# Kernel optimization log

Hardware: AMD Instinct MI355X
Metric: run time of the kernel (lower is better)

The kernel has to match this reference:

```python
import jax, jax.numpy as jnp
import numpy as np

NUM_CODES = 1024
CODE_DIM = 256
TEMPERATURE = 1.0  # forward default, clamped to >= 0.01 in original


def setup_inputs() -> dict:
    key = jax.random.key(0)
    k_z, k_e = jax.random.split(key)
    z = jax.random.normal(k_z, (16, 4096, CODE_DIM), dtype=jnp.float32)
    # embed buffer initialized as randn * 0.5 in the torch module
    embed = jax.random.normal(k_e, (NUM_CODES, CODE_DIM), dtype=jnp.float32) * 0.5
    return {"z": z, "embed": embed}


def reference(z, embed):
    K, D = embed.shape
    orig_shape = z.shape
    flat_z = z.reshape(-1, D)                      # [B, D]
    B = flat_z.shape[0]

    dist = (
        jnp.sum(flat_z * flat_z, axis=1, keepdims=True)
        - 2.0 * (flat_z @ embed.T)
        + jnp.sum(embed * embed, axis=1)[None, :]
    )

    soft_assign = jax.nn.softmax(-dist / max(TEMPERATURE, 0.01), axis=-1)  # [B, K]
    codes = jnp.argmin(dist, axis=1)               # [B]
    z_q = embed[codes]                             # [B, D] gather

    sg = jax.lax.stop_gradient
    commitment_loss = jnp.mean((flat_z - sg(z_q)) ** 2)
    codebook_loss = jnp.mean((z_q - sg(flat_z)) ** 2)

    avg_soft = jnp.mean(soft_assign, axis=0)       # [K]
    usage_entropy = -jnp.sum(avg_soft * jnp.log(avg_soft + 1e-10))
    diversity_loss = -usage_entropy / np.log(K).astype(np.float32)

    # straight-through estimator
    z_q_st = (flat_z + sg(z_q - flat_z)).reshape(orig_shape)
    codes_out = codes.reshape(orig_shape[:-1])

    # hard usage / perplexity (scatter-add instead of BxK one-hot)
    counts = jnp.zeros((K,), dtype=jnp.float32).at[codes].add(1.0)
    hard_avg = counts / jnp.asarray(B, dtype=jnp.float32)
    perplexity = jnp.exp(-jnp.sum(hard_avg * jnp.log(hard_avg + 1e-10)))

    return (z_q_st, codes_out, commitment_loss, codebook_loss,
            diversity_loss, usage_entropy, perplexity)
```

## Files before the change

kernel.cpp:

```cpp
#include <hip/hip_runtime.h>
#include <math.h>

typedef _Float16 half8 __attribute__((ext_vector_type(8)));
typedef float f32x4 __attribute__((ext_vector_type(4)));

#define AS1 __attribute__((address_space(1)))
#define AS3 __attribute__((address_space(3)))

#define BTOT   65536
#define DDIM   256
#define KC     1024

__global__ void vq_e2(const float* __restrict__ embed, float* __restrict__ e2g) {
    int gt = blockIdx.x * blockDim.x + threadIdx.x;
    int k = gt >> 6;
    int lane = gt & 63;
    float4 v = *(const float4*)(embed + (size_t)k * DDIM + lane * 4);
    float s = v.x * v.x + v.y * v.y + v.z * v.z + v.w * v.w;
    #pragma unroll
    for (int off = 1; off < 64; off <<= 1) s += __shfl_xor(s, off);
    if (lane == 0) e2g[k] = s;
}

__global__ void vq_prep(const float* __restrict__ embed, char* __restrict__ wsB) {
    int id = blockIdx.x * 256 + threadIdx.x;
    int c  = id >> 5;
    int kc = (id >> 2) & 7;
    int s  = id & 3;
    const float* src = embed + (size_t)c * DDIM + kc * 32 + s * 8;
    half8 hi, lo;
    #pragma unroll
    for (int j = 0; j < 8; ++j) {
        float xv = src[j];
        _Float16 hh = (_Float16)xv;
        hi[j] = hh;
        lo[j] = (_Float16)(xv - (float)hh);
    }
    int h = c >> 9, cl = c & 511;
    int inner = cl * 64 + ((s ^ (c & 3)) << 4);
    *(half8*)(wsB + (size_t)(kc * 4 + h) * 32768 + inner) = hi;
    *(half8*)(wsB + (size_t)(kc * 4 + 2 + h) * 32768 + inner) = lo;
}

__global__ __launch_bounds__(512, 2)
void vq_main(const float* __restrict__ z, const char* __restrict__ wsB,
             const float* __restrict__ e2g, float* __restrict__ psum_g,
             float* __restrict__ counts_g, float* __restrict__ distsum_g,
             float* __restrict__ codes_f_out)
{
    __shared__ __align__(16) char ldsA[65536];
    __shared__ __align__(16) char ldsB[2][32768];
    __shared__ float psum_lds[KC];
    __shared__ float lmax[64][8];
    __shared__ int   larg[64][8];
    __shared__ float lsum[64][8];
    __shared__ float rowM[64];
    __shared__ float rowInv[64];
    __shared__ float z2row[64];

    const int tid  = threadIdx.x;
    const int w    = tid >> 6;
    const int lane = tid & 63;
    const int row0 = blockIdx.x * 64;
    const int bA = (lane & 15) * 64 + (((lane >> 4) ^ (lane & 3)) << 4);

    psum_lds[tid] = 0.f;
    psum_lds[tid + 512] = 0.f;

    {
        const int ar = tid >> 3;
        const int kc = tid & 7;
        const float* src = z + (size_t)(row0 + ar) * DDIM + kc * 32;
        float x[32];
        #pragma unroll
        for (int j = 0; j < 8; ++j) {
            float4 v = ((const float4*)src)[j];
            x[4*j] = v.x; x[4*j+1] = v.y; x[4*j+2] = v.z; x[4*j+3] = v.w;
        }
        float zsq = 0.f;
        #pragma unroll
        for (int j = 0; j < 32; ++j) zsq = fmaf(x[j], x[j], zsq);
        zsq += __shfl_xor(zsq, 1);
        zsq += __shfl_xor(zsq, 2);
        zsq += __shfl_xor(zsq, 4);
        if ((tid & 7) == 0) z2row[ar] = zsq;
        #pragma unroll
        for (int s = 0; s < 4; ++s) {
            half8 hi, lo;
            #pragma unroll
            for (int j = 0; j < 8; ++j) {
                float xv = x[8*s + j];
                _Float16 hh = (_Float16)xv;
                hi[j] = hh;
                lo[j] = (_Float16)(xv - (float)hh);
            }
            int off = kc * 4096 + ar * 64 + ((s ^ (ar & 3)) << 4);
            *(half8*)(ldsA + off) = hi;
            *(half8*)(ldsA + 32768 + off) = lo;
        }
    }
    {
        const char* gs = wsB + tid * 16;
        char* ld = &ldsB[0][tid * 16];
        #pragma unroll
        for (int r = 0; r < 4; ++r)
            __builtin_amdgcn_global_load_lds((AS1 const void*)(gs + r * 8192),
                                             (AS3 void*)(ld + r * 8192), 16, 0, 0);
    }
    __syncthreads();

    f32x4 acc[4][8];
    #pragma unroll
    for (int rt = 0; rt < 4; ++rt)
        #pragma unroll
        for (int cg = 0; cg < 8; ++cg)
            acc[rt][cg] = (f32x4){0.f, 0.f, 0.f, 0.f};

    half8 aHi[4], aLo[4];

    #pragma unroll
    for (int kc = 0; kc < 8; ++kc) {
        #pragma unroll
        for (int p = 0; p < 2; ++p) {
            #pragma unroll
            for (int h = 0; h < 2; ++h) {
                const int s = kc * 4 + p * 2 + h;
                asm volatile("s_waitcnt vmcnt(0)\n\ts_barrier" ::: "memory");
                if (s + 1 < 32) {
                    const char* gs = wsB + (size_t)(s + 1) * 32768 + tid * 16;
                    char* ld = &ldsB[(s + 1) & 1][tid * 16];
                    #pragma unroll
                    for (int r = 0; r < 4; ++r)
                        __builtin_amdgcn_global_load_lds((AS1 const void*)(gs + r * 8192),
                                                         (AS3 void*)(ld + r * 8192), 16, 0, 0);
                }
                if (p == 0 && h == 0) {
                    #pragma unroll
                    for (int rt = 0; rt < 4; ++rt) {
                        aHi[rt] = *(const half8*)(ldsA + kc * 4096 + rt * 1024 + bA);
                        aLo[rt] = *(const half8*)(ldsA + 32768 + kc * 4096 + rt * 1024 + bA);
                    }
                }
                const char* bb = &ldsB[s & 1][w * 4096 + bA];
                #pragma unroll
                for (int ct = 0; ct < 4; ++ct) {
                    half8 bf = *(const half8*)(bb + ct * 1024);
                    const int cg = h * 4 + ct;
                    #pragma unroll
                    for (int rt = 0; rt < 4; ++rt) {
                        acc[rt][cg] = __builtin_amdgcn_mfma_f32_16x16x32_f16(
                            aHi[rt], bf, acc[rt][cg], 0, 0, 0);
                        if (p == 0)
                            acc[rt][cg] = __builtin_amdgcn_mfma_f32_16x16x32_f16(
                                aLo[rt], bf, acc[rt][cg], 0, 0, 0);
                    }
                }
            }
        }
    }

    int colv[8];
    float e2v[8];
    #pragma unroll
    for (int cg = 0; cg < 8; ++cg) {
        int colbase = (cg < 4) ? (w * 64 + cg * 16) : (512 + w * 64 + (cg - 4) * 16);
        colv[cg] = colbase + (lane & 15);
        e2v[cg] = e2g[colv[cg]];
    }
    #pragma unroll
    for (int rt = 0; rt < 4; ++rt) {
        #pragma unroll
        for (int i = 0; i < 4; ++i) {
            float m = -INFINITY; int am = 0x7fffffff;
            #pragma unroll
            for (int cg = 0; cg < 8; ++cg) {
                float l = fmaf(2.f, acc[rt][cg][i], -e2v[cg]);
                if (l > m) { m = l; am = colv[cg]; }
            }
            #pragma unroll
            for (int off = 1; off < 16; off <<= 1) {
                float om = __shfl_xor(m, off);
                int   oa = __shfl_xor(am, off);
                if (om > m || (om == m && oa < am)) { m = om; am = oa; }
            }
            if ((lane & 15) == 0) {
                int r = rt * 16 + ((lane >> 4) << 2) + i;
                lmax[r][w] = m; larg[r][w] = am;
            }
        }
    }
    __syncthreads();
    if (tid < 64) {
        float M = -INFINITY; int A = 0x7fffffff;
        #pragma unroll
        for (int ww = 0; ww < 8; ++ww) {
            float mm = lmax[tid][ww]; int aa = larg[tid][ww];
            if (mm > M || (mm == M && aa < A)) { M = mm; A = aa; }
        }
        rowM[tid] = M;
        codes_f_out[row0 + tid] = (float)A;
        atomicAdd(&counts_g[A], 1.0f);
        float d = z2row[tid] - M;
        #pragma unroll
        for (int off = 1; off < 64; off <<= 1) d += __shfl_xor(d, off);
        if (tid == 0) atomicAdd(distsum_g, d);
    }
    __syncthreads();
    #pragma unroll
    for (int rt = 0; rt < 4; ++rt) {
        #pragma unroll
        for (int i = 0; i < 4; ++i) {
            const int r = rt * 16 + ((lane >> 4) << 2) + i;
            float M = rowM[r];
            float ss = 0.f;
            #pragma unroll
            for (int cg = 0; cg < 8; ++cg) {
                float e = __expf(fmaf(2.f, acc[rt][cg][i], -e2v[cg]) - M);
                acc[rt][cg][i] = e;
                ss += e;
            }
            #pragma unroll
            for (int off = 1; off < 16; off <<= 1) ss += __shfl_xor(ss, off);
            if ((lane & 15) == 0) lsum[r][w] = ss;
        }
    }
    __syncthreads();
    if (tid < 64) {
        float S = 0.f;
        #pragma unroll
        for (int ww = 0; ww < 8; ++ww) S += lsum[tid][ww];
        rowInv[tid] = 1.0f / S;
    }
    __syncthreads();
    #pragma unroll
    for (int cg = 0; cg < 8; ++cg) {
        float cp = 0.f;
        #pragma unroll
        for (int rt = 0; rt < 4; ++rt)
            #pragma unroll
            for (int i = 0; i < 4; ++i)
                cp = fmaf(acc[rt][cg][i], rowInv[rt * 16 + ((lane >> 4) << 2) + i], cp);
        atomicAdd(&psum_lds[colv[cg]], cp);
    }
    __syncthreads();
    atomicAdd(&psum_g[tid], psum_lds[tid]);
    atomicAdd(&psum_g[tid + 512], psum_lds[tid + 512]);
}

__global__ void vq_gather(const float* __restrict__ embed,
                          const float* __restrict__ codes_f,
                          float* __restrict__ outq)
{
    int idx = blockIdx.x * 256 + threadIdx.x;
    int b = idx >> 6;
    int c = (int)codes_f[b];
    ((float4*)outq)[idx] = ((const float4*)embed)[(c << 6) + (idx & 63)];
}

__global__ void vq_finalize(const float* __restrict__ psum_g,
                            const float* __restrict__ counts_g,
                            const float* __restrict__ distsum_g,
                            float* __restrict__ out_s)
{
    __shared__ float s1[16], s2[16];
    int tid = threadIdx.x;
    float a = psum_g[tid] * (1.0f / 65536.0f);
    float e1 = -a * logf(a + 1e-10f);
    float h = counts_g[tid] * (1.0f / 65536.0f);
    float e2 = -h * logf(h + 1e-10f);
    #pragma unroll
    for (int off = 1; off < 64; off <<= 1) {
        e1 += __shfl_xor(e1, off);
        e2 += __shfl_xor(e2, off);
    }
    int w = tid >> 6, lane = tid & 63;
    if (lane == 0) { s1[w] = e1; s2[w] = e2; }
    __syncthreads();
    if (tid == 0) {
        float E1 = 0.0f, E2 = 0.0f;
        #pragma unroll
        for (int i = 0; i < 16; ++i) { E1 += s1[i]; E2 += s2[i]; }
        float commit = distsum_g[0] * (1.0f / 16777216.0f);
        out_s[0] = commit;
        out_s[1] = commit;
        out_s[2] = -E1 / 6.9314718055994531f;
        out_s[3] = E1;
        out_s[4] = __expf(E2);
    }
}

extern "C" void kernel_launch(void* const* d_in, const int* in_sizes, int n_in,
                              void* d_out, int out_size, void* d_ws, size_t ws_size,
                              hipStream_t stream) {
    const float* z     = (const float*)d_in[0];
    const float* embed = (const float*)d_in[1];

    float* out      = (float*)d_out;
    float* zq_out   = out;
    float* codes_f  = out + 16777216;
    float* scalars  = out + 16842752;

    float* ws        = (float*)d_ws;
    float* psum_g    = ws;
    float* counts_g  = ws + 1024;
    float* e2g       = ws + 2048;
    float* distsum_g = ws + 3072;
    char*  wsB       = (char*)d_ws + 16384;

    hipMemsetAsync(d_ws, 0, 3080 * sizeof(float), stream);
    vq_prep<<<128, 256, 0, stream>>>(embed, wsB);
    vq_e2<<<256, 256, 0, stream>>>(embed, e2g);
    vq_main<<<BTOT / 64, 512, 0, stream>>>(z, wsB, e2g, psum_g, counts_g,
                                           distsum_g, codes_f);
    vq_gather<<<4194304 / 256, 256, 0, stream>>>(embed, codes_f, zq_out);
    vq_finalize<<<1, 1024, 0, stream>>>(psum_g, counts_g, distsum_g, scalars);
}
```

Baseline: 202.1 us.

## Deepen B-tile pipeline to four 16KB stages and alias epilogue LDS

```diff
diff --git a/kernel.cpp b/kernel.cpp
--- a/kernel.cpp
+++ b/kernel.cpp
@@ -36,10 +36,10 @@
         hi[j] = hh;
         lo[j] = (_Float16)(xv - (float)hh);
     }
-    int h = c >> 9, cl = c & 511;
-    int inner = cl * 64 + ((s ^ (c & 3)) << 4);
-    *(half8*)(wsB + (size_t)(kc * 4 + h) * 32768 + inner) = hi;
-    *(half8*)(wsB + (size_t)(kc * 4 + 2 + h) * 32768 + inner) = lo;
+    int q = c >> 8, cl = c & 255;
+    int inner = cl * 64 + ((s ^ ((cl >> 1) & 3)) << 4);
+    *(half8*)(wsB + (size_t)(kc * 8 + q) * 16384 + inner) = hi;
+    *(half8*)(wsB + (size_t)(kc * 8 + 4 + q) * 16384 + inner) = lo;
 }
 
 __global__ __launch_bounds__(512, 2)
@@ -49,23 +49,30 @@
              float* __restrict__ codes_f_out)
 {
     __shared__ __align__(16) char ldsA[65536];
-    __shared__ __align__(16) char ldsB[2][32768];
-    __shared__ float psum_lds[KC];
-    __shared__ float lmax[64][8];
-    __shared__ int   larg[64][8];
-    __shared__ float lsum[64][8];
-    __shared__ float rowM[64];
-    __shared__ float rowInv[64];
-    __shared__ float z2row[64];
+    __shared__ __align__(16) char ldsBraw[65536];
+    float* lmax     = (float*)ldsBraw;
+    int*   larg     = (int*)(ldsBraw + 2048);
+    float* lsum     = (float*)(ldsBraw + 4096);
+    float* rowM     = (float*)(ldsBraw + 6144);
+    float* rowInv   = (float*)(ldsBraw + 6400);
+    float* psum_lds = (float*)(ldsBraw + 8192);
 
     const int tid  = threadIdx.x;
     const int w    = tid >> 6;
     const int lane = tid & 63;
     const int row0 = blockIdx.x * 64;
-    const int bA = (lane & 15) * 64 + (((lane >> 4) ^ (lane & 3)) << 4);
-
-    psum_lds[tid] = 0.f;
-    psum_lds[tid + 512] = 0.f;
+    const int swz   = ((lane >> 4) ^ ((lane >> 1) & 3)) << 4;
+    const int aBase = (lane & 15) * 64 + swz;
+    const int bBase = w * 2048 + (lane & 15) * 64 + swz;
+
+    #pragma unroll
+    for (int ps = 0; ps < 3; ++ps) {
+        const char* gs = wsB + (size_t)ps * 16384 + tid * 16;
+        char* ld = ldsBraw + ps * 16384 + tid * 16;
+        __builtin_amdgcn_global_load_lds((AS1 const void*)gs, (AS3 void*)ld, 16, 0, 0);
+        __builtin_amdgcn_global_load_lds((AS1 const void*)(gs + 8192),
+                                         (AS3 void*)(ld + 8192), 16, 0, 0);
+    }
 
     {
         const int ar = tid >> 3;
@@ -80,10 +87,9 @@
         float zsq = 0.f;
         #pragma unroll
         for (int j = 0; j < 32; ++j) zsq = fmaf(x[j], x[j], zsq);
-        zsq += __shfl_xor(zsq, 1);
-        zsq += __shfl_xor(zsq, 2);
-        zsq += __shfl_xor(zsq, 4);
-        if ((tid & 7) == 0) z2row[ar] = zsq;
+        #pragma unroll
+        for (int off = 1; off < 64; off <<= 1) zsq += __shfl_xor(zsq, off);
+        if (lane == 0) atomicAdd(distsum_g, zsq);
         #pragma unroll
         for (int s = 0; s < 4; ++s) {
             half8 hi, lo;
@@ -94,19 +100,11 @@
                 hi[j] = hh;
                 lo[j] = (_Float16)(xv - (float)hh);
             }
-            int off = kc * 4096 + ar * 64 + ((s ^ (ar & 3)) << 4);
+            int off = kc * 4096 + ar * 64 + ((s ^ ((ar >> 1) & 3)) << 4);
             *(half8*)(ldsA + off) = hi;
             *(half8*)(ldsA + 32768 + off) = lo;
         }
     }
-    {
-        const char* gs = wsB + tid * 16;
-        char* ld = &ldsB[0][tid * 16];
-        #pragma unroll
-        for (int r = 0; r < 4; ++r)
-            __builtin_amdgcn_global_load_lds((AS1 const void*)(gs + r * 8192),
-                                             (AS3 void*)(ld + r * 8192), 16, 0, 0);
-    }
     __syncthreads();
 
     f32x4 acc[4][8];
@@ -119,54 +117,51 @@
     half8 aHi[4], aLo[4];
 
     #pragma unroll
-    for (int kc = 0; kc < 8; ++kc) {
-        #pragma unroll
-        for (int p = 0; p < 2; ++p) {
-            #pragma unroll
-            for (int h = 0; h < 2; ++h) {
-                const int s = kc * 4 + p * 2 + h;
-                asm volatile("s_waitcnt vmcnt(0)\n\ts_barrier" ::: "memory");
-                if (s + 1 < 32) {
-                    const char* gs = wsB + (size_t)(s + 1) * 32768 + tid * 16;
-                    char* ld = &ldsB[(s + 1) & 1][tid * 16];
-                    #pragma unroll
-                    for (int r = 0; r < 4; ++r)
-                        __builtin_amdgcn_global_load_lds((AS1 const void*)(gs + r * 8192),
-                                                         (AS3 void*)(ld + r * 8192), 16, 0, 0);
-                }
-                if (p == 0 && h == 0) {
-                    #pragma unroll
-                    for (int rt = 0; rt < 4; ++rt) {
-                        aHi[rt] = *(const half8*)(ldsA + kc * 4096 + rt * 1024 + bA);
-                        aLo[rt] = *(const half8*)(ldsA + 32768 + kc * 4096 + rt * 1024 + bA);
-                    }
-                }
-                const char* bb = &ldsB[s & 1][w * 4096 + bA];
-                #pragma unroll
-                for (int ct = 0; ct < 4; ++ct) {
-                    half8 bf = *(const half8*)(bb + ct * 1024);
-                    const int cg = h * 4 + ct;
-                    #pragma unroll
-                    for (int rt = 0; rt < 4; ++rt) {
-                        acc[rt][cg] = __builtin_amdgcn_mfma_f32_16x16x32_f16(
-                            aHi[rt], bf, acc[rt][cg], 0, 0, 0);
-                        if (p == 0)
-                            acc[rt][cg] = __builtin_amdgcn_mfma_f32_16x16x32_f16(
-                                aLo[rt], bf, acc[rt][cg], 0, 0, 0);
-                    }
-                }
-            }
-        }
-    }
+    for (int s = 0; s < 64; ++s) {
+        const int kc = s >> 3, p = (s >> 2) & 1, q = s & 3;
+        if (s < 62)      asm volatile("s_waitcnt vmcnt(4)\n\ts_barrier" ::: "memory");
+        else if (s == 62) asm volatile("s_waitcnt vmcnt(2)\n\ts_barrier" ::: "memory");
+        else              asm volatile("s_waitcnt vmcnt(0)\n\ts_barrier" ::: "memory");
+        if (s + 3 < 64) {
+            const char* gs = wsB + (size_t)(s + 3) * 16384 + tid * 16;
+            char* ld = ldsBraw + ((s + 3) & 3) * 16384 + tid * 16;
+            __builtin_amdgcn_global_load_lds((AS1 const void*)gs, (AS3 void*)ld, 16, 0, 0);
+            __builtin_amdgcn_global_load_lds((AS1 const void*)(gs + 8192),
+                                             (AS3 void*)(ld + 8192), 16, 0, 0);
+        }
+        if (p == 0 && q == 0) {
+            #pragma unroll
+            for (int rt = 0; rt < 4; ++rt) {
+                aHi[rt] = *(const half8*)(ldsA + kc * 4096 + rt * 1024 + aBase);
+                aLo[rt] = *(const half8*)(ldsA + 32768 + kc * 4096 + rt * 1024 + aBase);
+            }
+        }
+        const char* bb = ldsBraw + (s & 3) * 16384 + bBase;
+        #pragma unroll
+        for (int ct = 0; ct < 2; ++ct) {
+            half8 bf = *(const half8*)(bb + ct * 1024);
+            const int cg = q * 2 + ct;
+            #pragma unroll
+            for (int rt = 0; rt < 4; ++rt) {
+                acc[rt][cg] = __builtin_amdgcn_mfma_f32_16x16x32_f16(
+                    aHi[rt], bf, acc[rt][cg], 0, 0, 0);
+                if (p == 0)
+                    acc[rt][cg] = __builtin_amdgcn_mfma_f32_16x16x32_f16(
+                        aLo[rt], bf, acc[rt][cg], 0, 0, 0);
+            }
+        }
+    }
+    __syncthreads();
 
     int colv[8];
     float e2v[8];
     #pragma unroll
     for (int cg = 0; cg < 8; ++cg) {
-        int colbase = (cg < 4) ? (w * 64 + cg * 16) : (512 + w * 64 + (cg - 4) * 16);
-        colv[cg] = colbase + (lane & 15);
+        colv[cg] = (cg >> 1) * 256 + w * 32 + (cg & 1) * 16 + (lane & 15);
         e2v[cg] = e2g[colv[cg]];
     }
+    psum_lds[tid] = 0.f;
+    psum_lds[tid + 512] = 0.f;
     #pragma unroll
     for (int rt = 0; rt < 4; ++rt) {
         #pragma unroll
@@ -185,7 +180,7 @@
             }
             if ((lane & 15) == 0) {
                 int r = rt * 16 + ((lane >> 4) << 2) + i;
-                lmax[r][w] = m; larg[r][w] = am;
+                lmax[r * 8 + w] = m; larg[r * 8 + w] = am;
             }
         }
     }
@@ -194,16 +189,16 @@
         float M = -INFINITY; int A = 0x7fffffff;
         #pragma unroll
         for (int ww = 0; ww < 8; ++ww) {
-            float mm = lmax[tid][ww]; int aa = larg[tid][ww];
+            float mm = lmax[tid * 8 + ww]; int aa = larg[tid * 8 + ww];
             if (mm > M || (mm == M && aa < A)) { M = mm; A = aa; }
         }
         rowM[tid] = M;
         codes_f_out[row0 + tid] = (float)A;
         atomicAdd(&counts_g[A], 1.0f);
-        float d = z2row[tid] - M;
-        #pragma unroll
-        for (int off = 1; off < 64; off <<= 1) d += __shfl_xor(d, off);
-        if (tid == 0) atomicAdd(distsum_g, d);
+        float negm = -M;
+        #pragma unroll
+        for (int off = 1; off < 64; off <<= 1) negm += __shfl_xor(negm, off);
+        if (tid == 0) atomicAdd(distsum_g, negm);
     }
     __syncthreads();
     #pragma unroll
@@ -221,14 +216,14 @@
             }
             #pragma unroll
             for (int off = 1; off < 16; off <<= 1) ss += __shfl_xor(ss, off);
-            if ((lane & 15) == 0) lsum[r][w] = ss;
+            if ((lane & 15) == 0) lsum[r * 8 + w] = ss;
         }
     }
     __syncthreads();
     if (tid < 64) {
         float S = 0.f;
         #pragma unroll
-        for (int ww = 0; ww < 8; ++ww) S += lsum[tid][ww];
+        for (int ww = 0; ww < 8; ++ww) S += lsum[tid * 8 + ww];
         rowInv[tid] = 1.0f / S;
     }
     __syncthreads();
```

Measured after the change: 224.4 us. +11.0%, slower.
